# Optimization experiments

Hardware: AMD Instinct MI355X
Metric: run time of the kernel (lower is better)

## Reference

```python
import jax, jax.numpy as jnp
import numpy as np

L, B, S, H = 24, 32, 512, 1024   # layers, batch, pad_size, bert hidden
D_IN, D1, D2 = L * H, 900, 40     # 24576 -> 900 -> 40 -> 1


def setup_inputs() -> dict:
    key = jax.random.key(0)
    ks = jax.random.split(key, 8)
    hidden_states = jax.random.normal(ks[0], (L, B, S, H), dtype=jnp.float32)
    # monotonically increasing subword start indices; 0 == "no word starts here"
    bert_token_starts = jnp.sort(
        jax.random.randint(ks[1], (B, S), 0, S, dtype=jnp.int64), axis=-1)
    W1 = jax.random.normal(ks[2], (D_IN, D1), dtype=jnp.float32) * 0.02
    b1 = jnp.zeros((D1,), dtype=jnp.float32)
    W2 = jax.random.normal(ks[3], (D1, D2), dtype=jnp.float32) * 0.02
    b2 = jnp.zeros((D2,), dtype=jnp.float32)
    W3 = jax.random.normal(ks[4], (D2, 1), dtype=jnp.float32) * 0.02
    b3 = jnp.zeros((1,), dtype=jnp.float32)
    return {
        "hidden_states": hidden_states,
        "W1": W1, "b1": b1, "W2": W2, "b2": b2, "W3": W3, "b3": b3,
        "bert_token_starts": bert_token_starts,
    }


def reference(hidden_states, W1, b1, W2, b2, W3, b3, bert_token_starts):
    # torch.cat over 24 layers along dim=2  ->  [B, S, 24*H] (layer-major feature order)
    x = jnp.moveaxis(hidden_states, 0, 2).reshape(
        hidden_states.shape[1], hidden_states.shape[2], -1)  # [B, S, 24576]
    h = jax.nn.relu(x @ W1 + b1)                # [B, S, 900]
    h = jax.nn.relu(h @ W2 + b2)                # [B, S, 40]
    pred_logits = jax.nn.sigmoid(h @ W3 + b3)[..., 0]  # squeeze(2) -> [B, S]
    # ragged gather: pred_labels[b][w] = pred_logits[b][starts[b][w]] where start != 0
    # (starts are always < pad_size here; the st/end while-loop in the original is dead code)
    valid = bert_token_starts != 0
    idx = jnp.clip(bert_token_starts, 0, pred_logits.shape[1] - 1)
    gathered = jnp.take_along_axis(pred_logits, idx, axis=1)
    pred_labels = jnp.where(valid, gathered, jnp.zeros((), dtype=pred_logits.dtype))
    return pred_labels
```

## Files before the change

### kernel.cpp

```cpp
#include <hip/hip_runtime.h>

typedef __attribute__((ext_vector_type(8))) short bf16x8;
typedef __attribute__((ext_vector_type(4))) float f32x4;

#define L_DIM 24
#define B_DIM 32
#define S_DIM 512
#define H_DIM 1024
#define M_DIM 16384
#define K_DIM 24576
#define N_REAL 900
#define NP 1024
#define BM 192

#define W1T_TILES 6144
#define SMALL_CHUNKS 164

__device__ __forceinline__ short f2bf(float f) {
  unsigned u = __builtin_bit_cast(unsigned, f);
  u += 0x7FFFu + ((u >> 16) & 1u);
  return (short)(u >> 16);
}
__device__ __forceinline__ float bflo(unsigned u) { return __builtin_bit_cast(float, u << 16); }
__device__ __forceinline__ float bfhi(unsigned u) { return __builtin_bit_cast(float, u & 0xffff0000u); }

__global__ __launch_bounds__(512)
void compact1_kernel(const int* __restrict__ starts, int* __restrict__ upos,
                     int* __restrict__ counts) {
  __shared__ int sc[512];
  const int b = blockIdx.x, t = threadIdx.x;
  const int v = starts[b * 512 + t];
  const int prev = (t > 0) ? starts[b * 512 + t - 1] : -1;
  const int flag = (v != 0 && v != prev) ? 1 : 0;
  sc[t] = flag;
  __syncthreads();
#pragma unroll
  for (int off = 1; off < 512; off <<= 1) {
    const int x = (t >= off) ? sc[t - off] : 0;
    __syncthreads();
    sc[t] += x;
    __syncthreads();
  }
  upos[b * 512 + t] = flag ? (sc[t] - 1) : -1;
  if (t == 511) counts[b] = sc[511];
}

__global__ __launch_bounds__(256)
void compact2_kernel(const int* __restrict__ counts, int* __restrict__ offs,
                     int* __restrict__ meta, int* __restrict__ idx) {
  __shared__ int s0, s1;
  if (threadIdx.x == 0) {
    int acc = 0;
    for (int b = 0; b < 32; ++b) { offs[b] = acc; acc += counts[b]; }
    const int pad = ((acc + BM - 1) / BM) * BM;
    meta[0] = acc;
    meta[1] = pad;
    s0 = acc; s1 = pad;
  }
  __syncthreads();
  for (int j = s0 + threadIdx.x; j < s1; j += 256) idx[j] = 0;
}

__global__ __launch_bounds__(512)
void compact3_kernel(const int* __restrict__ starts, const int* __restrict__ upos,
                     const int* __restrict__ offs, int* __restrict__ idx) {
  const int b = blockIdx.x, t = threadIdx.x;
  const int p = upos[b * 512 + t];
  if (p >= 0) idx[offs[b] + p] = b * 512 + starts[b * 512 + t];
}

__global__ __launch_bounds__(256)
void prep_fused_kernel(const float* __restrict__ hs, const int* __restrict__ idx,
                       const int* __restrict__ meta,
                       const float* __restrict__ w1, const float* __restrict__ w2,
                       const float* __restrict__ b1,
                       unsigned short* __restrict__ a,
                       unsigned short* __restrict__ w1t,
                       float* __restrict__ w2t, float* __restrict__ b1p) {
  __shared__ unsigned short t[64][72];
  const int mcp = meta[1];
  const int total = W1T_TILES + mcp + SMALL_CHUNKS;
  const int tid = threadIdx.x;

  for (int item = blockIdx.x; item < total; item += gridDim.x) {
    if (item < W1T_TILES) {
      const int n0 = (item & 15) * 64;
      const int k0 = (item >> 4) * 64;
      {
        const int nl = tid & 63;
        const int n = n0 + nl;
#pragma unroll
        for (int p = 0; p < 16; ++p) {
          const int kl = p * 4 + (tid >> 6);
          float v = (n < N_REAL) ? w1[(size_t)(k0 + kl) * N_REAL + n] : 0.f;
          t[nl][kl] = (unsigned short)f2bf(v);
        }
      }
      __syncthreads();
      {
        const int kl = tid & 63;
#pragma unroll
        for (int p = 0; p < 16; ++p) {
          const int nl2 = p * 4 + (tid >> 6);
          const int n = n0 + nl2;
          const int slot = ((kl >> 3) ^ (n & 7)) & 7;
          w1t[(size_t)n * K_DIM + k0 + slot * 8 + (kl & 7)] = t[nl2][kl];
        }
      }
      __syncthreads();
    } else if (item < W1T_TILES + mcp) {
      const int j = item - W1T_TILES;
      const int m = idx[j];
      const int b = m >> 9, s = m & 511;
      const int j7 = j & 7;
      unsigned short* dstRow = a + (size_t)j * K_DIM;
#pragma unroll
      for (int i = 0; i < 12; ++i) {
        const int g = tid + i * 256;
        const int l = g >> 7;
        const int h = (g & 127) * 8;
        const float* src = hs + (((size_t)l * B_DIM + b) * S_DIM + s) * H_DIM + h;
        float4 f0 = *(const float4*)src;
        float4 f1 = *(const float4*)(src + 4);
        bf16x8 p;
        p[0] = f2bf(f0.x); p[1] = f2bf(f0.y); p[2] = f2bf(f0.z); p[3] = f2bf(f0.w);
        p[4] = f2bf(f1.x); p[5] = f2bf(f1.y); p[6] = f2bf(f1.z); p[7] = f2bf(f1.w);
        const int slot = (g & 7) ^ j7;
        *(bf16x8*)(dstRow + (g & ~7) * 8 + slot * 8) = p;
      }
    } else {
      const int i = (item - W1T_TILES - mcp) * 256 + tid;
      if (i < 40 * NP) {
        const int jj = i >> 10, k = i & (NP - 1);
        w2t[i] = (k < N_REAL) ? w2[(size_t)k * 40 + jj] : 0.f;
      }
      const int t2 = i - 40 * NP;
      if (t2 >= 0 && t2 < NP)
        b1p[t2] = (t2 < N_REAL) ? b1[t2] : 0.f;
    }
  }
}

#define SBAR() do { __builtin_amdgcn_sched_barrier(0); __builtin_amdgcn_s_barrier(); __builtin_amdgcn_sched_barrier(0); } while (0)
#define WAIT_LGKM0() do { asm volatile("s_waitcnt lgkmcnt(0)" ::: "memory"); __builtin_amdgcn_sched_barrier(0); } while (0)
#define VMWAIT(N) do { asm volatile("s_waitcnt vmcnt(" #N ")" ::: "memory"); __builtin_amdgcn_sched_barrier(0); } while (0)

#define STAGE_A(DSTREG, TK) do {                                                       \
  _Pragma("unroll")                                                                    \
  for (int _i = 0; _i < 3; ++_i) {                                                     \
    const int _ch = wid * 3 + _i;                                                      \
    const int _row = _ch * 8 + (lane >> 3);                                            \
    __builtin_amdgcn_global_load_lds(                                                  \
      (const __attribute__((address_space(1))) void*)(a +                              \
          (size_t)(m0 + _row) * K_DIM + (TK) * 64 + (lane & 7) * 8),                   \
      (__attribute__((address_space(3))) void*)((DSTREG) + _ch * 1024),                \
      16, 0, 0);                                                                       \
  }                                                                                    \
} while (0)

#define STAGE_B(DSTREG, HALF, TK) do {                                                 \
  _Pragma("unroll")                                                                    \
  for (int _i = 0; _i < 2; ++_i) {                                                     \
    const int _ch = wid * 2 + _i;                                                      \
    const int _row = (HALF) * 128 + _ch * 8 + (lane >> 3);                             \
    __builtin_amdgcn_global_load_lds(                                                  \
      (const __attribute__((address_space(1))) void*)(w1t +                            \
          (size_t)(n0 + _row) * K_DIM + (TK) * 64 + (lane & 7) * 8),                   \
      (__attribute__((address_space(3))) void*)((DSTREG) + (HALF) * 16384 + _ch * 1024), \
      16, 0, 0);                                                                       \
  }                                                                                    \
} while (0)

#define LDA3(AV, MIBASE, ABUF) do {                                                    \
  _Pragma("unroll")                                                                    \
  for (int _mi = 0; _mi < 3; ++_mi) {                                                  \
    _Pragma("unroll")                                                                  \
    for (int _kk = 0; _kk < 2; ++_kk) {                                                \
      const int _r = ((MIBASE) / 3) * 96 + wr * 48 + _mi * 16 + r15;                   \
      AV[_mi][_kk] = *(const bf16x8*)((ABUF) + _r * 128 + (((_kk)*4 + hi4) ^ (_r & 7)) * 16); \
    }                                                                                  \
  }                                                                                    \
} while (0)

#define LDB2(BV, NIBASE, BBUF) do {                                                    \
  _Pragma("unroll")                                                                    \
  for (int _ni = 0; _ni < 2; ++_ni) {                                                  \
    _Pragma("unroll")                                                                  \
    for (int _kk = 0; _kk < 2; ++_kk) {                                                \
      const int _r = ((NIBASE) >> 1) * 128 + wc * 32 + _ni * 16 + r15;                 \
      BV[_ni][_kk] = *(const bf16x8*)((BBUF) + _r * 128 + (((_kk)*4 + hi4) ^ (_r & 7)) * 16); \
    }                                                                                  \
  }                                                                                    \
} while (0)

#define MFMA_Q(AV, BV, MIBASE, NIBASE) do {                                            \
  _Pragma("unroll")                                                                    \
  for (int _mi = 0; _mi < 3; ++_mi)                                                    \
    _Pragma("unroll")                                                                  \
    for (int _ni = 0; _ni < 2; ++_ni)                                                  \
      _Pragma("unroll")                                                                \
      for (int _kk = 0; _kk < 2; ++_kk)                                                \
        acc[(MIBASE) + _mi][(NIBASE) + _ni] = __builtin_amdgcn_mfma_f32_16x16x32_bf16( \
            AV[_mi][_kk], BV[_ni][_kk], acc[(MIBASE) + _mi][(NIBASE) + _ni], 0, 0, 0); \
} while (0)

#define TILE_BODY(T, AB, BB, ABN, BBN, S1, S2, S3, WAITSTMT) do {                      \
                                                       \
  LDA3(av, 0, (AB));                                                                   \
  LDB2(bv0, 0, (BB));                                                                  \
  if (S1) STAGE_A((ABN), (T) + 1);                                                     \
  SBAR();                                                                              \
  WAIT_LGKM0();                                                                        \
  __builtin_amdgcn_s_setprio(1);                                                       \
  MFMA_Q(av, bv0, 0, 0);                                                               \
  __builtin_amdgcn_s_setprio(0);                                                       \
  SBAR();                                                                              \
                                                       \
  LDB2(bv1, 2, (BB));                                                                  \
  if (S2) STAGE_B((BBN), 1, (T) + 1);                                                  \
  SBAR();                                                                              \
  WAIT_LGKM0();                                                                        \
  __builtin_amdgcn_s_setprio(1);                                                       \
  MFMA_Q(av, bv1, 0, 2);                                                               \
  __builtin_amdgcn_s_setprio(0);                                                       \
  SBAR();                                                                              \
                                                 \
  LDA3(av, 3, (AB));                                                                   \
  if (S3) STAGE_B((BB), 0, (T) + 2);                                                   \
  SBAR();                                                                              \
  WAIT_LGKM0();                                                                        \
  __builtin_amdgcn_s_setprio(1);                                                       \
  MFMA_Q(av, bv1, 3, 2);                                                               \
  MFMA_Q(av, bv0, 3, 0);                                                               \
  __builtin_amdgcn_s_setprio(0);                                                       \
  WAITSTMT;                                                                            \
  SBAR();                                                                              \
} while (0)

__global__ __launch_bounds__(512, 2)
void gemm1_192_kernel(const unsigned short* __restrict__ a,
                      const unsigned short* __restrict__ w1t,
                      const float* __restrict__ b1p,
                      const int* __restrict__ meta,
                      unsigned short* __restrict__ h1) {
  const int n_panels = meta[1] / BM;

  const int hw = blockIdx.x;
  const int c = hw & 7;
  const int r = hw >> 3;
  const int mb = (r >> 2) * 8 + c;
  if (mb >= n_panels) return;
  const int nb = r & 3;
  const int m0 = mb * BM;
  const int n0 = nb * 256;

  extern __shared__ char L[];
  char* const Ab0 = L;
  char* const Ab1 = L + 24576;
  char* const Bb0 = L + 49152;
  char* const Bb1 = L + 49152 + 32768;

  const int tid = threadIdx.x;
  const int lane = tid & 63;
  const int wid = tid >> 6;
  const int wr = wid >> 2;
  const int wc = wid & 3;
  const int r15 = lane & 15;
  const int hi4 = lane >> 4;

  f32x4 acc[6][4] = {};
  bf16x8 av[3][2], bv0[2][2], bv1[2][2];

  STAGE_B(Bb0, 0, 0);
  STAGE_A(Ab0, 0);
  STAGE_B(Bb0, 1, 0);
  STAGE_B(Bb1, 0, 1);
  VMWAIT(2);
  SBAR();

  for (int kt = 0; kt < 191; ++kt) {
    const int t = 2 * kt;
    TILE_BODY(t,     Ab0, Bb0, Ab1, Bb1, 1, 1, 1, VMWAIT(2));
    TILE_BODY(t + 1, Ab1, Bb1, Ab0, Bb0, 1, 1, 1, VMWAIT(2));
  }
  TILE_BODY(382, Ab0, Bb0, Ab1, Bb1, 1, 1, 0, VMWAIT(0));
  TILE_BODY(383, Ab1, Bb1, Ab0, Bb0, 0, 0, 0, (void)0);

#pragma unroll
  for (int mi = 0; mi < 6; ++mi) {
#pragma unroll
    for (int ni = 0; ni < 4; ++ni) {
      const int n = n0 + (ni >> 1) * 128 + wc * 32 + (ni & 1) * 16 + r15;
      const float bias = b1p[n];
#pragma unroll
      for (int rr = 0; rr < 4; ++rr) {
        const int m = m0 + (mi / 3) * 96 + wr * 48 + (mi % 3) * 16 + hi4 * 4 + rr;
        const float v = acc[mi][ni][rr] + bias;
        h1[(size_t)m * NP + n] = (unsigned short)f2bf(v > 0.f ? v : 0.f);
      }
    }
  }
}

__global__ __launch_bounds__(256)
void layer23_kernel(const unsigned short* __restrict__ h1, const float* __restrict__ w2t,
                    const float* __restrict__ b2, const float* __restrict__ w3,
                    const float* __restrict__ b3, const int* __restrict__ idx,
                    const int* __restrict__ meta, float* __restrict__ logits) {
  const int j = (blockIdx.x * 256 + threadIdx.x) >> 6;
  if (j >= meta[0]) return;
  const int lane = threadIdx.x & 63;
  const unsigned short* hrow = h1 + (size_t)j * NP;
  float acc = 0.f;
  if (lane < 40) {
    const float* wrow = w2t + lane * NP;
    for (int k = 0; k < NP; k += 8) {
      uint4 q = *(const uint4*)(hrow + k);
      float4 w0 = *(const float4*)(wrow + k);
      float4 w4 = *(const float4*)(wrow + k + 4);
      acc += bflo(q.x) * w0.x + bfhi(q.x) * w0.y;
      acc += bflo(q.y) * w0.z + bfhi(q.y) * w0.w;
      acc += bflo(q.z) * w4.x + bfhi(q.z) * w4.y;
      acc += bflo(q.w) * w4.z + bfhi(q.w) * w4.w;
    }
    acc += b2[lane];
    acc = acc > 0.f ? acc : 0.f;
    acc *= w3[lane];
  }
#pragma unroll
  for (int off = 32; off > 0; off >>= 1)
    acc += __shfl_down(acc, off);
  if (lane == 0)
    logits[idx[j]] = 1.f / (1.f + expf(-(acc + b3[0])));
}

__global__ __launch_bounds__(256)
void gather_kernel(const int* __restrict__ starts, const float* __restrict__ logits,
                   float* __restrict__ out) {
  const int i = blockIdx.x * 256 + threadIdx.x;
  if (i >= M_DIM) return;
  const int st = starts[i];
  int idx = st;
  if (idx < 0) idx = 0;
  if (idx > S_DIM - 1) idx = S_DIM - 1;
  out[i] = (st != 0) ? logits[((i >> 9) << 9) + idx] : 0.f;
}

extern "C" void kernel_launch(void* const* d_in, const int* in_sizes, int n_in,
                              void* d_out, int out_size, void* d_ws, size_t ws_size,
                              hipStream_t stream) {
  const float* hs = (const float*)d_in[0];
  const float* W1 = (const float*)d_in[1];
  const float* b1 = (const float*)d_in[2];
  const float* W2 = (const float*)d_in[3];
  const float* b2 = (const float*)d_in[4];
  const float* W3 = (const float*)d_in[5];
  const float* b3 = (const float*)d_in[6];
  const int* starts = (const int*)d_in[7];
  float* out = (float*)d_out;
  char* ws = (char*)d_ws;

  const size_t A_BYTES   = (size_t)(M_DIM + 256) * K_DIM * 2;
  const size_t W1T_BYTES = (size_t)NP * K_DIM * 2;
  const size_t H1_BYTES  = (size_t)(M_DIM + 256) * NP * 2;
  const size_t W2T_BYTES = 40 * NP * 4;
  const size_t B1P_BYTES = NP * 4;
  const size_t LG_BYTES  = M_DIM * 4;

  unsigned short* a    = (unsigned short*)ws;
  unsigned short* w1t  = (unsigned short*)(ws + A_BYTES);
  char* h1c            = ws + A_BYTES + W1T_BYTES;
  unsigned short* h1   = (unsigned short*)h1c;
  float* w2t           = (float*)(ws + A_BYTES + W1T_BYTES + H1_BYTES);
  float* b1p           = (float*)(ws + A_BYTES + W1T_BYTES + H1_BYTES + W2T_BYTES);
  float* logits        = (float*)(ws + A_BYTES + W1T_BYTES + H1_BYTES + W2T_BYTES + B1P_BYTES);
  int* idx             = (int*)(ws + A_BYTES + W1T_BYTES + H1_BYTES + W2T_BYTES + B1P_BYTES + LG_BYTES);
  int* meta            = (int*)(ws + A_BYTES + W1T_BYTES + H1_BYTES + W2T_BYTES + B1P_BYTES + LG_BYTES + 66560);
  int* upos            = (int*)h1c;
  int* counts          = (int*)(h1c + 65536);
  int* offs            = (int*)(h1c + 65536 + 128);

  hipFuncSetAttribute((const void*)gemm1_192_kernel,
                      hipFuncAttributeMaxDynamicSharedMemorySize, 114688);

  compact1_kernel<<<32, 512, 0, stream>>>(starts, upos, counts);
  compact2_kernel<<<1, 256, 0, stream>>>(counts, offs, meta, idx);
  compact3_kernel<<<32, 512, 0, stream>>>(starts, upos, offs, idx);
  prep_fused_kernel<<<4096, 256, 0, stream>>>(hs, idx, meta, W1, W2, b1,
                                              a, w1t, w2t, b1p);
  gemm1_192_kernel<<<352, 512, 114688, stream>>>(a, w1t, b1p, meta, h1);
  layer23_kernel<<<4096, 256, 0, stream>>>(h1, w2t, b2, W3, b3, idx, meta, logits);
  gather_kernel<<<64, 256, 0, stream>>>(starts, logits, out);
}
```

Baseline: 1.039 ms.

## Triple-buffer A tiles in GEMM1 to prefetch two K-steps ahead

Adds a third LDS buffer for the A operand and issues A loads two tiles ahead instead of one, rotating buffers across a 6-tile unrolled loop. The vmcnt waits are split and retuned so global loads have more time in flight, hiding memory latency behind MFMA work. Dynamic LDS grows from 112KB to 136KB. Occupancy should be unaffected, since two blocks per CU already exceeded the LDS budget. It does add code size and makes the buffer-rotation and wait bookkeeping more fragile.

```diff
diff --git a/kernel.cpp b/kernel.cpp
--- a/kernel.cpp
+++ b/kernel.cpp
@@ -204,20 +204,21 @@
             AV[_mi][_kk], BV[_ni][_kk], acc[(MIBASE) + _mi][(NIBASE) + _ni], 0, 0, 0); \
 } while (0)
 
-#define TILE_BODY(T, AB, BB, ABN, BBN, S1, S2, S3, WAITSTMT) do {                      \
+#define TILE_BODY(T, AB, BB, A2B, BBN, SA, SBB, SBA, W1STMT, W3STMT) do {              \
                                                        \
   LDA3(av, 0, (AB));                                                                   \
   LDB2(bv0, 0, (BB));                                                                  \
-  if (S1) STAGE_A((ABN), (T) + 1);                                                     \
+  if (SA) STAGE_A((A2B), (T) + 2);                                                     \
   SBAR();                                                                              \
   WAIT_LGKM0();                                                                        \
   __builtin_amdgcn_s_setprio(1);                                                       \
   MFMA_Q(av, bv0, 0, 0);                                                               \
   __builtin_amdgcn_s_setprio(0);                                                       \
+  W1STMT;                                                                              \
   SBAR();                                                                              \
                                                        \
   LDB2(bv1, 2, (BB));                                                                  \
-  if (S2) STAGE_B((BBN), 1, (T) + 1);                                                  \
+  if (SBB) STAGE_B((BBN), 1, (T) + 1);                                                 \
   SBAR();                                                                              \
   WAIT_LGKM0();                                                                        \
   __builtin_amdgcn_s_setprio(1);                                                       \
@@ -226,14 +227,14 @@
   SBAR();                                                                              \
                                                  \
   LDA3(av, 3, (AB));                                                                   \
-  if (S3) STAGE_B((BB), 0, (T) + 2);                                                   \
+  if (SBA) STAGE_B((BB), 0, (T) + 2);                                                  \
   SBAR();                                                                              \
   WAIT_LGKM0();                                                                        \
   __builtin_amdgcn_s_setprio(1);                                                       \
   MFMA_Q(av, bv1, 3, 2);                                                               \
   MFMA_Q(av, bv0, 3, 0);                                                               \
   __builtin_amdgcn_s_setprio(0);                                                       \
-  WAITSTMT;                                                                            \
+  W3STMT;                                                                              \
   SBAR();                                                                              \
 } while (0)
 
@@ -257,8 +258,9 @@
   extern __shared__ char L[];
   char* const Ab0 = L;
   char* const Ab1 = L + 24576;
-  char* const Bb0 = L + 49152;
-  char* const Bb1 = L + 49152 + 32768;
+  char* const Ab2 = L + 49152;
+  char* const Bq0 = L + 73728;
+  char* const Bq1 = L + 106496;
 
   const int tid = threadIdx.x;
   const int lane = tid & 63;
@@ -271,20 +273,29 @@
   f32x4 acc[6][4] = {};
   bf16x8 av[3][2], bv0[2][2], bv1[2][2];
 
-  STAGE_B(Bb0, 0, 0);
   STAGE_A(Ab0, 0);
-  STAGE_B(Bb0, 1, 0);
-  STAGE_B(Bb1, 0, 1);
-  VMWAIT(2);
+  STAGE_B(Bq0, 0, 0);
+  STAGE_A(Ab1, 1);
+  STAGE_B(Bq0, 1, 0);
+  STAGE_B(Bq1, 0, 1);
+  VMWAIT(7);
   SBAR();
 
-  for (int kt = 0; kt < 191; ++kt) {
-    const int t = 2 * kt;
-    TILE_BODY(t,     Ab0, Bb0, Ab1, Bb1, 1, 1, 1, VMWAIT(2));
-    TILE_BODY(t + 1, Ab1, Bb1, Ab0, Bb0, 1, 1, 1, VMWAIT(2));
-  }
-  TILE_BODY(382, Ab0, Bb0, Ab1, Bb1, 1, 1, 0, VMWAIT(0));
-  TILE_BODY(383, Ab1, Bb1, Ab0, Bb0, 0, 0, 0, (void)0);
+  for (int kt = 0; kt < 63; ++kt) {
+    const int t = 6 * kt;
+    TILE_BODY(t + 0, Ab0, Bq0, Ab2, Bq1, 1, 1, 1, VMWAIT(5), VMWAIT(7));
+    TILE_BODY(t + 1, Ab1, Bq1, Ab0, Bq0, 1, 1, 1, VMWAIT(5), VMWAIT(7));
+    TILE_BODY(t + 2, Ab2, Bq0, Ab1, Bq1, 1, 1, 1, VMWAIT(5), VMWAIT(7));
+    TILE_BODY(t + 3, Ab0, Bq1, Ab2, Bq0, 1, 1, 1, VMWAIT(5), VMWAIT(7));
+    TILE_BODY(t + 4, Ab1, Bq0, Ab0, Bq1, 1, 1, 1, VMWAIT(5), VMWAIT(7));
+    TILE_BODY(t + 5, Ab2, Bq1, Ab1, Bq0, 1, 1, 1, VMWAIT(5), VMWAIT(7));
+  }
+  TILE_BODY(378, Ab0, Bq0, Ab2, Bq1, 1, 1, 1, VMWAIT(5), VMWAIT(7));
+  TILE_BODY(379, Ab1, Bq1, Ab0, Bq0, 1, 1, 1, VMWAIT(5), VMWAIT(7));
+  TILE_BODY(380, Ab2, Bq0, Ab1, Bq1, 1, 1, 1, VMWAIT(5), VMWAIT(7));
+  TILE_BODY(381, Ab0, Bq1, Ab2, Bq0, 1, 1, 1, VMWAIT(5), VMWAIT(7));
+  TILE_BODY(382, Ab1, Bq0, Ab2, Bq1, 0, 1, 0, VMWAIT(2), VMWAIT(2));
+  TILE_BODY(383, Ab2, Bq1, Ab0, Bq0, 0, 0, 0, VMWAIT(0), (void)0);
 
 #pragma unroll
   for (int mi = 0; mi < 6; ++mi) {
@@ -381,14 +392,14 @@
   int* offs            = (int*)(h1c + 65536 + 128);
 
   hipFuncSetAttribute((const void*)gemm1_192_kernel,
-                      hipFuncAttributeMaxDynamicSharedMemorySize, 114688);
+                      hipFuncAttributeMaxDynamicSharedMemorySize, 139264);
 
   compact1_kernel<<<32, 512, 0, stream>>>(starts, upos, counts);
   compact2_kernel<<<1, 256, 0, stream>>>(counts, offs, meta, idx);
   compact3_kernel<<<32, 512, 0, stream>>>(starts, upos, offs, idx);
   prep_fused_kernel<<<4096, 256, 0, stream>>>(hs, idx, meta, W1, W2, b1,
                                               a, w1t, w2t, b1p);
-  gemm1_192_kernel<<<352, 512, 114688, stream>>>(a, w1t, b1p, meta, h1);
+  gemm1_192_kernel<<<352, 512, 139264, stream>>>(a, w1t, b1p, meta, h1);
   layer23_kernel<<<4096, 256, 0, stream>>>(h1, w2t, b2, W3, b3, idx, meta, logits);
   gather_kernel<<<64, 256, 0, stream>>>(starts, logits, out);
 }
```

New measurement: 1.018 ms. 1.02x faster.

## Shrink GEMM1 tile to 192x128 with 4 waves and 8 column blocks

Applied to the files above, without the earlier changes.

Reshapes the first-layer GEMM from 192x256 tiles on 8 waves to 192x128 tiles on 4 waves. Each wave now stages twice as many A chunks, and the vmcnt waits are retuned for the new load counts. The N dimension is split into 8 column blocks and the grid grows to 448 workgroups with less LDS each. The aim is more workgroups and better occupancy and load balance across CUs. The cost is that each A tile is re-read by twice as many column blocks, doubling A traffic, and the reduced wave count may hurt latency hiding.

```diff
diff --git a/kernel.cpp b/kernel.cpp
--- a/kernel.cpp
+++ b/kernel.cpp
@@ -12,6 +12,7 @@
 #define N_REAL 900
 #define NP 1024
 #define BM 192
+#define BN 128
 
 #define W1T_TILES 6144
 #define SMALL_CHUNKS 164
@@ -147,8 +148,8 @@
 
 #define STAGE_A(DSTREG, TK) do {                                                       \
   _Pragma("unroll")                                                                    \
-  for (int _i = 0; _i < 3; ++_i) {                                                     \
-    const int _ch = wid * 3 + _i;                                                      \
+  for (int _i = 0; _i < 6; ++_i) {                                                     \
+    const int _ch = wid * 6 + _i;                                                      \
     const int _row = _ch * 8 + (lane >> 3);                                            \
     __builtin_amdgcn_global_load_lds(                                                  \
       (const __attribute__((address_space(1))) void*)(a +                              \
@@ -162,11 +163,11 @@
   _Pragma("unroll")                                                                    \
   for (int _i = 0; _i < 2; ++_i) {                                                     \
     const int _ch = wid * 2 + _i;                                                      \
-    const int _row = (HALF) * 128 + _ch * 8 + (lane >> 3);                             \
+    const int _row = (HALF) * 64 + _ch * 8 + (lane >> 3);                              \
     __builtin_amdgcn_global_load_lds(                                                  \
       (const __attribute__((address_space(1))) void*)(w1t +                            \
           (size_t)(n0 + _row) * K_DIM + (TK) * 64 + (lane & 7) * 8),                   \
-      (__attribute__((address_space(3))) void*)((DSTREG) + (HALF) * 16384 + _ch * 1024), \
+      (__attribute__((address_space(3))) void*)((DSTREG) + (HALF) * 8192 + _ch * 1024), \
       16, 0, 0);                                                                       \
   }                                                                                    \
 } while (0)
@@ -187,7 +188,7 @@
   for (int _ni = 0; _ni < 2; ++_ni) {                                                  \
     _Pragma("unroll")                                                                  \
     for (int _kk = 0; _kk < 2; ++_kk) {                                                \
-      const int _r = ((NIBASE) >> 1) * 128 + wc * 32 + _ni * 16 + r15;                 \
+      const int _r = ((NIBASE) >> 1) * 64 + wc * 32 + _ni * 16 + r15;                  \
       BV[_ni][_kk] = *(const bf16x8*)((BBUF) + _r * 128 + (((_kk)*4 + hi4) ^ (_r & 7)) * 16); \
     }                                                                                  \
   }                                                                                    \
@@ -204,20 +205,21 @@
             AV[_mi][_kk], BV[_ni][_kk], acc[(MIBASE) + _mi][(NIBASE) + _ni], 0, 0, 0); \
 } while (0)
 
-#define TILE_BODY(T, AB, BB, ABN, BBN, S1, S2, S3, WAITSTMT) do {                      \
+#define TILE_BODY(T, AB, BB, ABN, BBN, SA, SBB, SBA, W1STMT, W3STMT) do {              \
                                                        \
   LDA3(av, 0, (AB));                                                                   \
   LDB2(bv0, 0, (BB));                                                                  \
-  if (S1) STAGE_A((ABN), (T) + 1);                                                     \
+  if (SA) STAGE_A((ABN), (T) + 1);                                                     \
   SBAR();                                                                              \
   WAIT_LGKM0();                                                                        \
   __builtin_amdgcn_s_setprio(1);                                                       \
   MFMA_Q(av, bv0, 0, 0);                                                               \
   __builtin_amdgcn_s_setprio(0);                                                       \
+  W1STMT;                                                                              \
   SBAR();                                                                              \
                                                        \
   LDB2(bv1, 2, (BB));                                                                  \
-  if (S2) STAGE_B((BBN), 1, (T) + 1);                                                  \
+  if (SBB) STAGE_B((BBN), 1, (T) + 1);                                                 \
   SBAR();                                                                              \
   WAIT_LGKM0();                                                                        \
   __builtin_amdgcn_s_setprio(1);                                                       \
@@ -226,18 +228,18 @@
   SBAR();                                                                              \
                                                  \
   LDA3(av, 3, (AB));                                                                   \
-  if (S3) STAGE_B((BB), 0, (T) + 2);                                                   \
+  if (SBA) STAGE_B((BB), 0, (T) + 2);                                                  \
   SBAR();                                                                              \
   WAIT_LGKM0();                                                                        \
   __builtin_amdgcn_s_setprio(1);                                                       \
   MFMA_Q(av, bv1, 3, 2);                                                               \
   MFMA_Q(av, bv0, 3, 0);                                                               \
   __builtin_amdgcn_s_setprio(0);                                                       \
-  WAITSTMT;                                                                            \
-  SBAR();                                                                              \
-} while (0)
-
-__global__ __launch_bounds__(512, 2)
+  W3STMT;                                                                              \
+  SBAR();                                                                              \
+} while (0)
+
+__global__ __launch_bounds__(256, 2)
 void gemm1_192_kernel(const unsigned short* __restrict__ a,
                       const unsigned short* __restrict__ w1t,
                       const float* __restrict__ b1p,
@@ -248,49 +250,49 @@
   const int hw = blockIdx.x;
   const int c = hw & 7;
   const int r = hw >> 3;
-  const int mb = (r >> 2) * 8 + c;
+  const int mb = (r >> 3) * 8 + c;
   if (mb >= n_panels) return;
-  const int nb = r & 3;
+  const int nb = r & 7;
   const int m0 = mb * BM;
-  const int n0 = nb * 256;
+  const int n0 = nb * BN;
 
   extern __shared__ char L[];
   char* const Ab0 = L;
   char* const Ab1 = L + 24576;
-  char* const Bb0 = L + 49152;
-  char* const Bb1 = L + 49152 + 32768;
+  char* const Bq0 = L + 49152;
+  char* const Bq1 = L + 65536;
 
   const int tid = threadIdx.x;
   const int lane = tid & 63;
   const int wid = tid >> 6;
-  const int wr = wid >> 2;
-  const int wc = wid & 3;
+  const int wr = wid >> 1;
+  const int wc = wid & 1;
   const int r15 = lane & 15;
   const int hi4 = lane >> 4;
 
   f32x4 acc[6][4] = {};
   bf16x8 av[3][2], bv0[2][2], bv1[2][2];
 
-  STAGE_B(Bb0, 0, 0);
   STAGE_A(Ab0, 0);
-  STAGE_B(Bb0, 1, 0);
-  STAGE_B(Bb1, 0, 1);
-  VMWAIT(2);
+  STAGE_B(Bq0, 0, 0);
+  STAGE_B(Bq0, 1, 0);
+  STAGE_B(Bq1, 0, 1);
+  VMWAIT(4);
   SBAR();
 
   for (int kt = 0; kt < 191; ++kt) {
     const int t = 2 * kt;
-    TILE_BODY(t,     Ab0, Bb0, Ab1, Bb1, 1, 1, 1, VMWAIT(2));
-    TILE_BODY(t + 1, Ab1, Bb1, Ab0, Bb0, 1, 1, 1, VMWAIT(2));
-  }
-  TILE_BODY(382, Ab0, Bb0, Ab1, Bb1, 1, 1, 0, VMWAIT(0));
-  TILE_BODY(383, Ab1, Bb1, Ab0, Bb0, 0, 0, 0, (void)0);
+    TILE_BODY(t,     Ab0, Bq0, Ab1, Bq1, 1, 1, 1, VMWAIT(8), VMWAIT(4));
+    TILE_BODY(t + 1, Ab1, Bq1, Ab0, Bq0, 1, 1, 1, VMWAIT(8), VMWAIT(4));
+  }
+  TILE_BODY(382, Ab0, Bq0, Ab1, Bq1, 0, 1, 0, VMWAIT(2), VMWAIT(2));
+  TILE_BODY(383, Ab1, Bq1, Ab0, Bq0, 0, 0, 0, VMWAIT(0), (void)0);
 
 #pragma unroll
   for (int mi = 0; mi < 6; ++mi) {
 #pragma unroll
     for (int ni = 0; ni < 4; ++ni) {
-      const int n = n0 + (ni >> 1) * 128 + wc * 32 + (ni & 1) * 16 + r15;
+      const int n = n0 + (ni >> 1) * 64 + wc * 32 + (ni & 1) * 16 + r15;
       const float bias = b1p[n];
 #pragma unroll
       for (int rr = 0; rr < 4; ++rr) {
@@ -381,14 +383,14 @@
   int* offs            = (int*)(h1c + 65536 + 128);
 
   hipFuncSetAttribute((const void*)gemm1_192_kernel,
-                      hipFuncAttributeMaxDynamicSharedMemorySize, 114688);
+                      hipFuncAttributeMaxDynamicSharedMemorySize, 81920);
 
   compact1_kernel<<<32, 512, 0, stream>>>(starts, upos, counts);
   compact2_kernel<<<1, 256, 0, stream>>>(counts, offs, meta, idx);
   compact3_kernel<<<32, 512, 0, stream>>>(starts, upos, offs, idx);
   prep_fused_kernel<<<4096, 256, 0, stream>>>(hs, idx, meta, W1, W2, b1,
                                               a, w1t, w2t, b1p);
-  gemm1_192_kernel<<<352, 512, 114688, stream>>>(a, w1t, b1p, meta, h1);
+  gemm1_192_kernel<<<448, 256, 81920, stream>>>(a, w1t, b1p, meta, h1);
   layer23_kernel<<<4096, 256, 0, stream>>>(h1, w2t, b2, W3, b3, idx, meta, logits);
   gather_kernel<<<64, 256, 0, stream>>>(starts, logits, out);
 }
```

Result: slower. 1.092 ms (+5.1%).
